# Kernel optimization log

Measured on AMD Instinct MI355X. Metric: run time of the kernel, lower is better.

Reference implementation:

```python
import jax, jax.numpy as jnp
import numpy as np

VOCAB, EMB, HID = 32000, 128, 256
BS, SEQ = 8, 1024


def setup_inputs() -> dict:
    key = jax.random.key(0)
    ks = jax.random.split(key, 6)
    return {
        "sentence": jax.random.randint(ks[0], (BS, SEQ), 0, VOCAB, dtype=jnp.int64 if jax.config.jax_enable_x64 else jnp.int32),
        "w_embedding": jax.random.normal(ks[1], (VOCAB, EMB), jnp.float32) * float(np.sqrt(2.0 / VOCAB)),
        "W": jax.random.normal(ks[2], (EMB, 4 * HID), jnp.float32) * float(np.sqrt(2.0 / EMB)),
        "U": jax.random.normal(ks[3], (HID, 4 * HID), jnp.float32) * float(np.sqrt(2.0 / HID)),
        "bias": jnp.zeros((4 * HID,), jnp.float32),
        "w_linear": jax.random.normal(ks[4], (HID, VOCAB), jnp.float32) * float(np.sqrt(2.0 / HID)),
        "bias_linear": jnp.zeros((VOCAB,), jnp.float32),
    }


def reference(sentence, w_embedding, W, U, bias, w_linear, bias_linear):
    HS = U.shape[0]
    x = jnp.take(w_embedding, sentence, axis=0)          # (bs, seq, emb)
    bs = x.shape[0]
    # precompute input contribution to gates for all timesteps at once
    xW = jnp.einsum('bse,eg->bsg', x, W) + bias          # (bs, seq, 4H)
    xW_t = jnp.transpose(xW, (1, 0, 2))                  # (seq, bs, 4H)

    def step(carry, xw):
        h, c = carry
        gates = xw + h @ U                               # (bs, 4H)
        i = jax.nn.sigmoid(gates[:, :HS])
        f = jax.nn.sigmoid(gates[:, HS:2 * HS])
        g = jnp.tanh(gates[:, 2 * HS:3 * HS])
        o = jax.nn.sigmoid(gates[:, 3 * HS:])
        c = f * c + i * g
        h = o * jnp.tanh(c)
        return (h, c), h

    h0 = jnp.zeros((bs, HS), x.dtype)
    c0 = jnp.zeros((bs, HS), x.dtype)
    _, hidden_seq = jax.lax.scan(step, (h0, c0), xW_t)   # (seq, bs, H)
    hidden_seq = jnp.transpose(hidden_seq, (1, 0, 2))    # (bs, seq, H)
    prob = jnp.einsum('bsh,hv->bsv', hidden_seq, w_linear) + bias_linear
    return prob
```

## Files before the change

kernel.cpp:

```cpp
#include <hip/hip_runtime.h>
#include <hip/hip_bf16.h>

#define VOCAB 32000
#define EMB   128
#define HID   256
#define G4H   1024
#define BS    8
#define SEQ   1024
#define NWG   8

typedef __attribute__((ext_vector_type(8))) short short8;
typedef __attribute__((ext_vector_type(4))) float f32x4;
typedef __attribute__((ext_vector_type(2))) int   i32x2;

static __device__ __forceinline__ unsigned short f2bf(float x) {
  union { __hip_bfloat16 b; unsigned short u; } cv;
  cv.b = __float2bfloat16(x);
  return cv.u;
}
static __device__ __forceinline__ float bf2f(unsigned short u) {
  union { unsigned short u; __hip_bfloat16 b; } cv;
  cv.u = u;
  return __bfloat162float(cv.b);
}

static __device__ __forceinline__ float fsigmoid(float x) {
  return 1.f / (1.f + __expf(-x));
}
static __device__ __forceinline__ float ftanh(float x) {
  return 2.f / (1.f + __expf(-2.f * x)) - 1.f;
}

static __device__ __forceinline__ int ld_int_cc(const int* p) {
  int r;
  asm volatile("global_load_dword %0, %1, off sc0 sc1\n\ts_waitcnt vmcnt(0)"
               : "=v"(r) : "v"(p) : "memory");
  return r;
}
static __device__ __forceinline__ void st_int_cc(int* p, int v) {
  asm volatile("global_store_dword %0, %1, off sc0 sc1" :: "v"(p), "v"(v) : "memory");
}
static __device__ __forceinline__ short8 ld16_cc(const unsigned short* p) {
  short8 r;
  asm volatile("global_load_dwordx4 %0, %1, off sc0 sc1" : "=v"(r) : "v"(p) : "memory");
  return r;
}
static __device__ __forceinline__ void st8_cc(unsigned short* p, i32x2 v) {
  asm volatile("global_store_dwordx2 %0, %1, off sc0 sc1" :: "v"(p), "v"(v) : "memory");
}

__global__ __launch_bounds__(256) void k_embed_xw(
    const int* __restrict__ sent, const float* __restrict__ wemb,
    const float* __restrict__ W, const float* __restrict__ bias,
    float* __restrict__ xW) {
  int tid = threadIdx.x;
  int blk = blockIdx.x;
  int b  = blk >> 8;
  int t0 = (blk & 255) << 2;
  __shared__ float xs[4][EMB];
  #pragma unroll
  for (int i = 0; i < 2; ++i) {
    int flat = tid + (i << 8);
    int r = flat >> 7, e = flat & 127;
    int idx = sent[b * SEQ + t0 + r];
    xs[r][e] = wemb[idx * EMB + e];
  }
  __syncthreads();
  int g0 = tid << 2;
  float acc[4][4] = {};
  for (int e = 0; e < EMB; ++e) {
    float4 w4 = *(const float4*)&W[e * G4H + g0];
    #pragma unroll
    for (int r = 0; r < 4; ++r) {
      float xv = xs[r][e];
      acc[r][0] += xv * w4.x; acc[r][1] += xv * w4.y;
      acc[r][2] += xv * w4.z; acc[r][3] += xv * w4.w;
    }
  }
  float4 bi = *(const float4*)&bias[g0];
  #pragma unroll
  for (int r = 0; r < 4; ++r) {
    float4 o;
    o.x = acc[r][0] + bi.x; o.y = acc[r][1] + bi.y;
    o.z = acc[r][2] + bi.z; o.w = acc[r][3] + bi.w;
    *(float4*)&xW[(size_t)(b * SEQ + t0 + r) * G4H + g0] = o;
  }
}

__global__ __launch_bounds__(256) void k_transpose_w(
    const float* __restrict__ w, unsigned short* __restrict__ BT) {
  __shared__ unsigned short tile[64][66];
  int n0 = blockIdx.x * 64, k0 = blockIdx.y * 64;
  int tid = threadIdx.x;
  #pragma unroll
  for (int i = 0; i < 16; ++i) {
    int flat = tid + i * 256;
    int kk = flat >> 6, nn = flat & 63;
    tile[kk][nn] = f2bf(w[(size_t)(k0 + kk) * VOCAB + n0 + nn]);
  }
  __syncthreads();
  #pragma unroll
  for (int i = 0; i < 16; ++i) {
    int flat = tid + i * 256;
    int nn = flat >> 6, kk = flat & 63;
    BT[(size_t)(n0 + nn) * HID + k0 + kk] = tile[kk][nn];
  }
}

__global__ __launch_bounds__(512) void k_scan(
    const float* __restrict__ xW, const float* __restrict__ U,
    unsigned short* __restrict__ hidden,
    unsigned short* __restrict__ hbuf,
    unsigned short* __restrict__ lbuf,
    int* __restrict__ flags) {
  const int w = blockIdx.x;
  const int tid = threadIdx.x;
  const int l = tid & 63, v = tid >> 6;
  const int Wv = w * 8 + v;

  const int c16 = l & 15;
  const int colU = (c16 & 3) * HID + Wv * 4 + (c16 >> 2);
  short8 bhi[8], blo[8];
  #pragma unroll
  for (int kb = 0; kb < 8; ++kb) {
    #pragma unroll
    for (int j = 0; j < 8; ++j) {
      int k = kb * 32 + (l >> 4) * 8 + j;
      float uv = U[k * G4H + colU];
      unsigned short h16 = f2bf(uv);
      bhi[kb][j] = (short)h16;
      blo[kb][j] = (short)f2bf(uv - bf2f(h16));
    }
  }

  const int bat = l & 7;
  const int hl  = (l >> 3) & 3;
  const int H   = Wv * 4 + hl;

  __shared__ float xh[8][4][16][4];
  __shared__ unsigned short hp[8][8][4];
  __shared__ unsigned short lp[8][8][4];

  float xwp[4];
  if (l < 32) {
    #pragma unroll
    for (int g = 0; g < 4; ++g)
      xwp[g] = xW[((size_t)bat * SEQ + 0) * G4H + g * HID + H];
  }

  float c = 0.f;
  for (int t = 0; t < SEQ; ++t) {
    float sg[4] = {0.f, 0.f, 0.f, 0.f};
    if (t > 0) {
      if (v == 0) {
        const int* fp = &flags[l & 7];
        int guard = 0;
        for (;;) {
          int f = ld_int_cc(fp);
          if (__all(f >= t)) break;
          if (++guard > 30000) break;
        }
      }
      __syncthreads();

      const unsigned short* hb = hbuf + ((t - 1) & 1) * 2048;
      const unsigned short* lb = lbuf + ((t - 1) & 1) * 2048;
      short8 ah[8], al[8];
      #pragma unroll
      for (int kb = 0; kb < 8; ++kb) {
        int off = ((kb * 4 + (l >> 4)) * 8 + (l & 7)) * 8;
        ah[kb] = ld16_cc(hb + off);
        al[kb] = ld16_cc(lb + off);
      }
      asm volatile("s_waitcnt vmcnt(0)" ::: "memory");
      __builtin_amdgcn_sched_barrier(0);
      f32x4 a1 = {0.f, 0.f, 0.f, 0.f};
      f32x4 a2 = {0.f, 0.f, 0.f, 0.f};
      f32x4 a3 = {0.f, 0.f, 0.f, 0.f};
      #pragma unroll
      for (int kb = 0; kb < 8; ++kb) {
        a1 = __builtin_amdgcn_mfma_f32_16x16x32_bf16(ah[kb], bhi[kb], a1, 0, 0, 0);
        a2 = __builtin_amdgcn_mfma_f32_16x16x32_bf16(ah[kb], blo[kb], a2, 0, 0, 0);
        a3 = __builtin_amdgcn_mfma_f32_16x16x32_bf16(al[kb], bhi[kb], a3, 0, 0, 0);
      }
      f32x4 acc = a1 + a2 + a3;
      *(f32x4*)&xh[v][l >> 4][c16][0] = acc;
      asm volatile("s_waitcnt lgkmcnt(0)" ::: "memory");
      __builtin_amdgcn_sched_barrier(0);
      if (l < 32) {
        #pragma unroll
        for (int g = 0; g < 4; ++g)
          sg[g] = xh[v][bat >> 2][hl * 4 + g][bat & 3];
      }
    }

    unsigned short hhi = 0;
    if (l < 32) {
      float iv = fsigmoid(sg[0] + xwp[0]);
      float fv = fsigmoid(sg[1] + xwp[1]);
      float gv = ftanh   (sg[2] + xwp[2]);
      float ov = fsigmoid(sg[3] + xwp[3]);
      c = fv * c + iv * gv;
      float h = ov * ftanh(c);
      hhi = f2bf(h);
      hp[v][bat][hl] = hhi;
      lp[v][bat][hl] = f2bf(h - bf2f(hhi));
    }
    asm volatile("s_waitcnt lgkmcnt(0)" ::: "memory");
    __builtin_amdgcn_sched_barrier(0);
    if (l < 8) {
      unsigned h0 = hp[v][l][0], h1 = hp[v][l][1], h2 = hp[v][l][2], h3 = hp[v][l][3];
      unsigned o0 = lp[v][l][0], o1 = lp[v][l][1], o2 = lp[v][l][2], o3 = lp[v][l][3];
      i32x2 rh, rl;
      rh.x = (int)((h1 << 16) | h0); rh.y = (int)((h3 << 16) | h2);
      rl.x = (int)((o1 << 16) | o0); rl.y = (int)((o3 << 16) | o2);
      int off = ((Wv >> 1) * 8 + l) * 8 + (Wv & 1) * 4;
      st8_cc(hbuf + (t & 1) * 2048 + off, rh);
      st8_cc(lbuf + (t & 1) * 2048 + off, rl);
    }
    asm volatile("s_waitcnt vmcnt(0)" ::: "memory");
    __syncthreads();
    if (tid == 0) st_int_cc(&flags[w], t + 1);
    if (l < 32) {
      hidden[((size_t)bat * SEQ + t) * HID + H] = hhi;
      int tn = (t + 1 < SEQ) ? t + 1 : t;
      #pragma unroll
      for (int g = 0; g < 4; ++g)
        xwp[g] = xW[((size_t)bat * SEQ + tn) * G4H + g * HID + H];
    }
  }
}

__global__ __launch_bounds__(256) void k_gemm_out(
    const unsigned short* __restrict__ A,
    const unsigned short* __restrict__ BT,
    const float* __restrict__ bias, float* __restrict__ C) {
  const int n0 = blockIdx.x * 128;
  const int m0 = blockIdx.y * 128;
  const int tid = threadIdx.x;
  const int l = tid & 63, wv = tid >> 6;
  const int wr = wv >> 1, wc = wv & 1;
  __shared__ unsigned short As[128 * 72];
  __shared__ unsigned short Bs[128 * 72];
  f32x4 acc[4][4] = {};
  const int r = tid >> 1, seg = tid & 1;
  for (int kt = 0; kt < 4; ++kt) {
    int k0 = kt * 64;
    #pragma unroll
    for (int i = 0; i < 4; ++i) {
      *(short8*)&As[r * 72 + seg * 32 + i * 8] =
          *(const short8*)&A[(size_t)(m0 + r) * HID + k0 + seg * 32 + i * 8];
      *(short8*)&Bs[r * 72 + seg * 32 + i * 8] =
          *(const short8*)&BT[(size_t)(n0 + r) * HID + k0 + seg * 32 + i * 8];
    }
    __syncthreads();
    #pragma unroll
    for (int kb = 0; kb < 2; ++kb) {
      short8 af[4], bf[4];
      #pragma unroll
      for (int mi = 0; mi < 4; ++mi)
        af[mi] = *(const short8*)&As[(wr * 64 + mi * 16 + (l & 15)) * 72 +
                                     kb * 32 + (l >> 4) * 8];
      #pragma unroll
      for (int ni = 0; ni < 4; ++ni)
        bf[ni] = *(const short8*)&Bs[(wc * 64 + ni * 16 + (l & 15)) * 72 +
                                     kb * 32 + (l >> 4) * 8];
      #pragma unroll
      for (int mi = 0; mi < 4; ++mi)
        #pragma unroll
        for (int ni = 0; ni < 4; ++ni)
          acc[mi][ni] = __builtin_amdgcn_mfma_f32_16x16x32_bf16(
              af[mi], bf[ni], acc[mi][ni], 0, 0, 0);
    }
    __syncthreads();
  }
  #pragma unroll
  for (int ni = 0; ni < 4; ++ni) {
    int n = n0 + wc * 64 + ni * 16 + (l & 15);
    float bi = bias[n];
    #pragma unroll
    for (int mi = 0; mi < 4; ++mi) {
      int mbase = m0 + wr * 64 + mi * 16 + (l >> 4) * 4;
      #pragma unroll
      for (int q = 0; q < 4; ++q)
        C[(size_t)(mbase + q) * VOCAB + n] = acc[mi][ni][q] + bi;
    }
  }
}

extern "C" void kernel_launch(void* const* d_in, const int* in_sizes, int n_in,
                              void* d_out, int out_size, void* d_ws, size_t ws_size,
                              hipStream_t stream) {
  const int*   sent = (const int*)d_in[0];
  const float* wemb = (const float*)d_in[1];
  const float* W    = (const float*)d_in[2];
  const float* U    = (const float*)d_in[3];
  const float* bias = (const float*)d_in[4];
  const float* wlin = (const float*)d_in[5];
  const float* blin = (const float*)d_in[6];
  float* out = (float*)d_out;

  float* xW = out;

  char* ws = (char*)d_ws;
  unsigned short* BT     = (unsigned short*)ws;
  unsigned short* hidden = (unsigned short*)(ws + 16384000);
  unsigned short* hbuf   = (unsigned short*)(ws + 16384000 + 4194304);
  unsigned short* lbuf   = (unsigned short*)(ws + 16384000 + 4194304 + 16384);
  int* flags             = (int*)(ws + 16384000 + 4194304 + 32768);

  hipMemsetAsync(flags, 0, 32, stream);
  k_embed_xw<<<2048, 256, 0, stream>>>(sent, wemb, W, bias, xW);
  k_transpose_w<<<dim3(500, 4), 256, 0, stream>>>(wlin, BT);
  k_scan<<<NWG, 512, 0, stream>>>(xW, U, hidden, hbuf, lbuf, flags);
  k_gemm_out<<<dim3(250, 64), 256, 0, stream>>>(hidden, BT, blin, out);
}
```

Before: 3.438 ms.

## Fuse LSTM scan with output GEMM via progress flags to overlap work

Merges the recurrent scan and the vocabulary projection GEMM into one persistent launch. The first 8 blocks run the scan and publish per-timestep progress counters. The remaining blocks wait on those counters and compute 128x256 output tiles as soon as their rows of hidden states exist, so the GEMM overlaps the latency-bound recurrence instead of running after it. The GEMM tile grows to 128x256 with 512 threads, and xW moves to the tail of the output buffer so early GEMM tiles do not overwrite it while the scan still reads it. This relies on the scan blocks being scheduled alongside thousands of spinning GEMM blocks, which adds deadlock and ordering risk, and tiles overlapping the xW region are held until the scan completes.

```diff
diff --git a/kernel.cpp b/kernel.cpp
--- a/kernel.cpp
+++ b/kernel.cpp
@@ -107,151 +107,196 @@
   }
 }
 
-__global__ __launch_bounds__(512) void k_scan(
+struct ScanS {
+  float xh[8][4][16][4];
+  unsigned short hp[8][8][4];
+  unsigned short lp[8][8][4];
+};
+struct GemmS {
+  unsigned short As[128 * 72];
+  unsigned short Bs[256 * 72];
+};
+union SMem { ScanS s; GemmS g; };
+
+__global__ __launch_bounds__(512) void k_fused(
     const float* __restrict__ xW, const float* __restrict__ U,
     unsigned short* __restrict__ hidden,
     unsigned short* __restrict__ hbuf,
     unsigned short* __restrict__ lbuf,
-    int* __restrict__ flags) {
-  const int w = blockIdx.x;
+    int* __restrict__ flags,
+    int* __restrict__ prog,
+    const unsigned short* __restrict__ BT,
+    const float* __restrict__ blin,
+    float* __restrict__ C) {
+  __shared__ SMem sm;
+  const int bx = blockIdx.x;
   const int tid = threadIdx.x;
   const int l = tid & 63, v = tid >> 6;
-  const int Wv = w * 8 + v;
-
-  const int c16 = l & 15;
-  const int colU = (c16 & 3) * HID + Wv * 4 + (c16 >> 2);
-  short8 bhi[8], blo[8];
-  #pragma unroll
-  for (int kb = 0; kb < 8; ++kb) {
-    #pragma unroll
-    for (int j = 0; j < 8; ++j) {
-      int k = kb * 32 + (l >> 4) * 8 + j;
-      float uv = U[k * G4H + colU];
-      unsigned short h16 = f2bf(uv);
-      bhi[kb][j] = (short)h16;
-      blo[kb][j] = (short)f2bf(uv - bf2f(h16));
-    }
-  }
-
-  const int bat = l & 7;
-  const int hl  = (l >> 3) & 3;
-  const int H   = Wv * 4 + hl;
-
-  __shared__ float xh[8][4][16][4];
-  __shared__ unsigned short hp[8][8][4];
-  __shared__ unsigned short lp[8][8][4];
-
-  float xwp[4];
-  if (l < 32) {
-    #pragma unroll
-    for (int g = 0; g < 4; ++g)
-      xwp[g] = xW[((size_t)bat * SEQ + 0) * G4H + g * HID + H];
-  }
-
-  float c = 0.f;
-  for (int t = 0; t < SEQ; ++t) {
-    float sg[4] = {0.f, 0.f, 0.f, 0.f};
-    if (t > 0) {
-      if (v == 0) {
-        const int* fp = &flags[l & 7];
-        int guard = 0;
-        for (;;) {
-          int f = ld_int_cc(fp);
-          if (__all(f >= t)) break;
-          if (++guard > 30000) break;
+
+  if (bx < NWG) {
+    const int w = bx;
+    const int Wv = w * 8 + v;
+
+    const int c16 = l & 15;
+    const int colU = (c16 & 3) * HID + Wv * 4 + (c16 >> 2);
+    short8 bhi[8], blo[8];
+    #pragma unroll
+    for (int kb = 0; kb < 8; ++kb) {
+      #pragma unroll
+      for (int j = 0; j < 8; ++j) {
+        int k = kb * 32 + (l >> 4) * 8 + j;
+        float uv = U[k * G4H + colU];
+        unsigned short h16 = f2bf(uv);
+        bhi[kb][j] = (short)h16;
+        blo[kb][j] = (short)f2bf(uv - bf2f(h16));
+      }
+    }
+
+    const int bat = l & 7;
+    const int hl  = (l >> 3) & 3;
+    const int H   = Wv * 4 + hl;
+
+    float xwp[4];
+    if (l < 32) {
+      #pragma unroll
+      for (int g = 0; g < 4; ++g)
+        xwp[g] = xW[((size_t)bat * SEQ + 0) * G4H + g * HID + H];
+    }
+
+    float c = 0.f;
+    for (int t = 0; t < SEQ; ++t) {
+      float sg[4] = {0.f, 0.f, 0.f, 0.f};
+      if (t > 0) {
+        if (v == 0) {
+          const int* fp = &flags[l & 7];
+          int guard = 0;
+          for (;;) {
+            int f = ld_int_cc(fp);
+            if (__all(f >= t)) break;
+            if (++guard > 30000) break;
+          }
+          if (w == 0 && l < 8) st_int_cc(&prog[l * 16], t);
         }
-      }
-      __syncthreads();
-
-      const unsigned short* hb = hbuf + ((t - 1) & 1) * 2048;
-      const unsigned short* lb = lbuf + ((t - 1) & 1) * 2048;
-      short8 ah[8], al[8];
-      #pragma unroll
-      for (int kb = 0; kb < 8; ++kb) {
-        int off = ((kb * 4 + (l >> 4)) * 8 + (l & 7)) * 8;
-        ah[kb] = ld16_cc(hb + off);
-        al[kb] = ld16_cc(lb + off);
-      }
-      asm volatile("s_waitcnt vmcnt(0)" ::: "memory");
-      __builtin_amdgcn_sched_barrier(0);
-      f32x4 a1 = {0.f, 0.f, 0.f, 0.f};
-      f32x4 a2 = {0.f, 0.f, 0.f, 0.f};
-      f32x4 a3 = {0.f, 0.f, 0.f, 0.f};
-      #pragma unroll
-      for (int kb = 0; kb < 8; ++kb) {
-        a1 = __builtin_amdgcn_mfma_f32_16x16x32_bf16(ah[kb], bhi[kb], a1, 0, 0, 0);
-        a2 = __builtin_amdgcn_mfma_f32_16x16x32_bf16(ah[kb], blo[kb], a2, 0, 0, 0);
-        a3 = __builtin_amdgcn_mfma_f32_16x16x32_bf16(al[kb], bhi[kb], a3, 0, 0, 0);
-      }
-      f32x4 acc = a1 + a2 + a3;
-      *(f32x4*)&xh[v][l >> 4][c16][0] = acc;
+        __syncthreads();
+
+        const unsigned short* hb = hbuf + ((t - 1) & 1) * 2048;
+        const unsigned short* lb = lbuf + ((t - 1) & 1) * 2048;
+        short8 ah[8], al[8];
+        #pragma unroll
+        for (int kb = 0; kb < 8; ++kb) {
+          int off = ((kb * 4 + (l >> 4)) * 8 + (l & 7)) * 8;
+          ah[kb] = ld16_cc(hb + off);
+          al[kb] = ld16_cc(lb + off);
+        }
+        asm volatile("s_waitcnt vmcnt(0)" ::: "memory");
+        __builtin_amdgcn_sched_barrier(0);
+        f32x4 a1 = {0.f, 0.f, 0.f, 0.f};
+        f32x4 a2 = {0.f, 0.f, 0.f, 0.f};
+        f32x4 a3 = {0.f, 0.f, 0.f, 0.f};
+        #pragma unroll
+        for (int kb = 0; kb < 8; ++kb) {
+          a1 = __builtin_amdgcn_mfma_f32_16x16x32_bf16(ah[kb], bhi[kb], a1, 0, 0, 0);
+          a2 = __builtin_amdgcn_mfma_f32_16x16x32_bf16(ah[kb], blo[kb], a2, 0, 0, 0);
+          a3 = __builtin_amdgcn_mfma_f32_16x16x32_bf16(al[kb], bhi[kb], a3, 0, 0, 0);
+        }
+        f32x4 acc = a1 + a2 + a3;
+        *(f32x4*)&sm.s.xh[v][l >> 4][c16][0] = acc;
+        asm volatile("s_waitcnt lgkmcnt(0)" ::: "memory");
+        __builtin_amdgcn_sched_barrier(0);
+        if (l < 32) {
+          #pragma unroll
+          for (int g = 0; g < 4; ++g)
+            sg[g] = sm.s.xh[v][bat >> 2][hl * 4 + g][bat & 3];
+        }
+      }
+
+      if (l < 32) {
+        float iv = fsigmoid(sg[0] + xwp[0]);
+        float fv = fsigmoid(sg[1] + xwp[1]);
+        float gv = ftanh   (sg[2] + xwp[2]);
+        float ov = fsigmoid(sg[3] + xwp[3]);
+        c = fv * c + iv * gv;
+        float h = ov * ftanh(c);
+        unsigned short hhi = f2bf(h);
+        sm.s.hp[v][bat][hl] = hhi;
+        sm.s.lp[v][bat][hl] = f2bf(h - bf2f(hhi));
+      }
       asm volatile("s_waitcnt lgkmcnt(0)" ::: "memory");
       __builtin_amdgcn_sched_barrier(0);
+      if (l < 8) {
+        unsigned h0 = sm.s.hp[v][l][0], h1 = sm.s.hp[v][l][1];
+        unsigned h2 = sm.s.hp[v][l][2], h3 = sm.s.hp[v][l][3];
+        unsigned o0 = sm.s.lp[v][l][0], o1 = sm.s.lp[v][l][1];
+        unsigned o2 = sm.s.lp[v][l][2], o3 = sm.s.lp[v][l][3];
+        i32x2 rh, rl;
+        rh.x = (int)((h1 << 16) | h0); rh.y = (int)((h3 << 16) | h2);
+        rl.x = (int)((o1 << 16) | o0); rl.y = (int)((o3 << 16) | o2);
+        int off = ((Wv >> 1) * 8 + l) * 8 + (Wv & 1) * 4;
+        st8_cc(hbuf + (t & 1) * 2048 + off, rh);
+        st8_cc(lbuf + (t & 1) * 2048 + off, rl);
+        st8_cc(hidden + ((size_t)l * SEQ + t) * HID + Wv * 4, rh);
+      }
+      asm volatile("s_waitcnt vmcnt(0)" ::: "memory");
+      __syncthreads();
+      if (tid == 0) st_int_cc(&flags[w], t + 1);
       if (l < 32) {
+        int tn = (t + 1 < SEQ) ? t + 1 : t;
         #pragma unroll
         for (int g = 0; g < 4; ++g)
-          sg[g] = xh[v][bat >> 2][hl * 4 + g][bat & 3];
-      }
-    }
-
-    unsigned short hhi = 0;
-    if (l < 32) {
-      float iv = fsigmoid(sg[0] + xwp[0]);
-      float fv = fsigmoid(sg[1] + xwp[1]);
-      float gv = ftanh   (sg[2] + xwp[2]);
-      float ov = fsigmoid(sg[3] + xwp[3]);
-      c = fv * c + iv * gv;
-      float h = ov * ftanh(c);
-      hhi = f2bf(h);
-      hp[v][bat][hl] = hhi;
-      lp[v][bat][hl] = f2bf(h - bf2f(hhi));
-    }
-    asm volatile("s_waitcnt lgkmcnt(0)" ::: "memory");
-    __builtin_amdgcn_sched_barrier(0);
-    if (l < 8) {
-      unsigned h0 = hp[v][l][0], h1 = hp[v][l][1], h2 = hp[v][l][2], h3 = hp[v][l][3];
-      unsigned o0 = lp[v][l][0], o1 = lp[v][l][1], o2 = lp[v][l][2], o3 = lp[v][l][3];
-      i32x2 rh, rl;
-      rh.x = (int)((h1 << 16) | h0); rh.y = (int)((h3 << 16) | h2);
-      rl.x = (int)((o1 << 16) | o0); rl.y = (int)((o3 << 16) | o2);
-      int off = ((Wv >> 1) * 8 + l) * 8 + (Wv & 1) * 4;
-      st8_cc(hbuf + (t & 1) * 2048 + off, rh);
-      st8_cc(lbuf + (t & 1) * 2048 + off, rl);
-    }
-    asm volatile("s_waitcnt vmcnt(0)" ::: "memory");
-    __syncthreads();
-    if (tid == 0) st_int_cc(&flags[w], t + 1);
-    if (l < 32) {
-      hidden[((size_t)bat * SEQ + t) * HID + H] = hhi;
-      int tn = (t + 1 < SEQ) ? t + 1 : t;
-      #pragma unroll
-      for (int g = 0; g < 4; ++g)
-        xwp[g] = xW[((size_t)bat * SEQ + tn) * G4H + g * HID + H];
-    }
-  }
-}
-
-__global__ __launch_bounds__(256) void k_gemm_out(
-    const unsigned short* __restrict__ A,
-    const unsigned short* __restrict__ BT,
-    const float* __restrict__ bias, float* __restrict__ C) {
-  const int n0 = blockIdx.x * 128;
-  const int m0 = blockIdx.y * 128;
-  const int tid = threadIdx.x;
-  const int l = tid & 63, wv = tid >> 6;
-  const int wr = wv >> 1, wc = wv & 1;
-  __shared__ unsigned short As[128 * 72];
-  __shared__ unsigned short Bs[128 * 72];
+          xwp[g] = xW[((size_t)bat * SEQ + tn) * G4H + g * HID + H];
+      }
+    }
+    if (bx == 0 && v == 0) {
+      const int* fp = &flags[l & 7];
+      int guard = 0;
+      for (;;) {
+        int f = ld_int_cc(fp);
+        if (__all(f >= SEQ)) break;
+        if (++guard > 30000) break;
+      }
+      if (l < 8) st_int_cc(&prog[l * 16], SEQ);
+    }
+    return;
+  }
+
+  const int gb = bx - NWG;
+  int nb = gb % 125;
+  int t2 = gb / 125;
+  int bat = t2 & 7, tblk = t2 >> 3;
+  int m0 = bat * 1024 + tblk * 128;
+  int n0 = nb * 256;
+  int gate = (bat == 7 && tblk >= 5) ? SEQ : (tblk * 128 + 128);
+
+  if (tid == 0) {
+    const int* pp = &prog[(gb & 7) * 16];
+    int guard = 0;
+    while (ld_int_cc(pp) < gate) {
+      __builtin_amdgcn_s_sleep(64);
+      if (++guard > 1000000) break;
+    }
+  }
+  __syncthreads();
+
+  const unsigned short* A = hidden;
+  const int g  = v >> 2;
+  const int wq = v & 3;
+  const int wr = wq >> 1, wc = wq & 1;
   f32x4 acc[4][4] = {};
-  const int r = tid >> 1, seg = tid & 1;
   for (int kt = 0; kt < 4; ++kt) {
     int k0 = kt * 64;
     #pragma unroll
+    for (int i = 0; i < 2; ++i) {
+      int flat = tid + i * 512;
+      int r = flat >> 3, cc = flat & 7;
+      *(short8*)&sm.g.As[r * 72 + cc * 8] =
+          *(const short8*)&A[(size_t)(m0 + r) * HID + k0 + cc * 8];
+    }
+    #pragma unroll
     for (int i = 0; i < 4; ++i) {
-      *(short8*)&As[r * 72 + seg * 32 + i * 8] =
-          *(const short8*)&A[(size_t)(m0 + r) * HID + k0 + seg * 32 + i * 8];
-      *(short8*)&Bs[r * 72 + seg * 32 + i * 8] =
-          *(const short8*)&BT[(size_t)(n0 + r) * HID + k0 + seg * 32 + i * 8];
+      int flat = tid + i * 512;
+      int r = flat >> 3, cc = flat & 7;
+      *(short8*)&sm.g.Bs[r * 72 + cc * 8] =
+          *(const short8*)&BT[(size_t)(n0 + r) * HID + k0 + cc * 8];
     }
     __syncthreads();
     #pragma unroll
@@ -259,12 +304,12 @@
       short8 af[4], bf[4];
       #pragma unroll
       for (int mi = 0; mi < 4; ++mi)
-        af[mi] = *(const short8*)&As[(wr * 64 + mi * 16 + (l & 15)) * 72 +
-                                     kb * 32 + (l >> 4) * 8];
+        af[mi] = *(const short8*)&sm.g.As[(wr * 64 + mi * 16 + (l & 15)) * 72 +
+                                          kb * 32 + (l >> 4) * 8];
       #pragma unroll
       for (int ni = 0; ni < 4; ++ni)
-        bf[ni] = *(const short8*)&Bs[(wc * 64 + ni * 16 + (l & 15)) * 72 +
-                                     kb * 32 + (l >> 4) * 8];
+        bf[ni] = *(const short8*)&sm.g.Bs[(g * 128 + wc * 64 + ni * 16 + (l & 15)) * 72 +
+                                          kb * 32 + (l >> 4) * 8];
       #pragma unroll
       for (int mi = 0; mi < 4; ++mi)
         #pragma unroll
@@ -276,8 +321,8 @@
   }
   #pragma unroll
   for (int ni = 0; ni < 4; ++ni) {
-    int n = n0 + wc * 64 + ni * 16 + (l & 15);
-    float bi = bias[n];
+    int n = n0 + g * 128 + wc * 64 + ni * 16 + (l & 15);
+    float bi = blin[n];
     #pragma unroll
     for (int mi = 0; mi < 4; ++mi) {
       int mbase = m0 + wr * 64 + mi * 16 + (l >> 4) * 4;
@@ -300,7 +345,7 @@
   const float* blin = (const float*)d_in[6];
   float* out = (float*)d_out;
 
-  float* xW = out;
+  float* xW = out + (262144000 - 8388608);
 
   char* ws = (char*)d_ws;
   unsigned short* BT     = (unsigned short*)ws;
@@ -308,10 +353,11 @@
   unsigned short* hbuf   = (unsigned short*)(ws + 16384000 + 4194304);
   unsigned short* lbuf   = (unsigned short*)(ws + 16384000 + 4194304 + 16384);
   int* flags             = (int*)(ws + 16384000 + 4194304 + 32768);
-
-  hipMemsetAsync(flags, 0, 32, stream);
+  int* prog              = (int*)(ws + 16384000 + 4194304 + 32768 + 64);
+
+  hipMemsetAsync(flags, 0, 64 + 512, stream);
   k_embed_xw<<<2048, 256, 0, stream>>>(sent, wemb, W, bias, xW);
   k_transpose_w<<<dim3(500, 4), 256, 0, stream>>>(wlin, BT);
-  k_scan<<<NWG, 512, 0, stream>>>(xW, U, hidden, hbuf, lbuf, flags);
-  k_gemm_out<<<dim3(250, 64), 256, 0, stream>>>(hidden, BT, blin, out);
-}
+  k_fused<<<NWG + 8000, 512, 0, stream>>>(xW, U, hidden, hbuf, lbuf,
+                                          flags, prog, BT, blin, out);
+}
```

After: 3.456 ms. Within noise of the previous version (+0.5%).
